# Kernel optimization log

Measured on AMD Instinct MI355X. Metric: run time of the kernel, lower is better.

The kernel has to match this reference:

```python
import jax, jax.numpy as jnp
import numpy as np

B, N, C = 64, 197, 768
H = 12
N_TOK = 118
CUTOFF = 0.15


def setup_inputs() -> dict:
    key = jax.random.key(0)
    ks = jax.random.split(key, 6)
    s = 0.02
    return {
        "x": jax.random.normal(ks[0], (B, N, C), jnp.float32),
        "ln1_w": jnp.ones((C,), jnp.float32),
        "ln1_b": jnp.zeros((C,), jnp.float32),
        "qkv_w": jax.random.normal(ks[1], (3 * C, C), jnp.float32) * s,
        "proj_w": jax.random.normal(ks[2], (C, C), jnp.float32) * s,
        "proj_b": jnp.zeros((C,), jnp.float32),
        "gamma1": jnp.ones((C,), jnp.float32),
        "ln2_w": jnp.ones((C,), jnp.float32),
        "ln2_b": jnp.zeros((C,), jnp.float32),
        "fc1_w": jax.random.normal(ks[3], (4 * C, C), jnp.float32) * s,
        "fc1_b": jnp.zeros((4 * C,), jnp.float32),
        "fc2_w": jax.random.normal(ks[4], (C, 4 * C), jnp.float32) * s,
        "fc2_b": jnp.zeros((C,), jnp.float32),
        "gamma2": jnp.ones((C,), jnp.float32),
    }


def _ln(x, w, b, eps=1e-5):
    m = x.mean(-1, keepdims=True)
    v = ((x - m) ** 2).mean(-1, keepdims=True)
    return (x - m) / jnp.sqrt(v + eps) * w + b


def _attention(x, qkv_w, proj_w, proj_b):
    Bx, Nx, Cx = x.shape
    dh = Cx // H
    qkv = x @ qkv_w.T                                    # [B,N,3C]
    qk = qkv[:, :, : 2 * Cx].reshape(Bx, Nx, 2, H, dh).transpose(2, 0, 3, 1, 4)
    q, k = qk[0], qk[1]                                  # [B,H,N,dh]
    v = qkv[:, :, 2 * Cx :].reshape(Bx, Nx, H, dh).transpose(0, 2, 1, 3)
    attn = jax.nn.softmax((q * dh ** -0.5) @ k.transpose(0, 1, 3, 2), axis=-1)  # [B,H,N,N]
    out = (attn @ v).transpose(0, 2, 1, 3).reshape(Bx, Nx, Cx)
    return out @ proj_w.T + proj_b, attn


def _selector(x, attn, n_tokens, cutoff):
    # attention-weighted scores
    cls_aw = attn[:, :, 1:, 0].mean(-1)[..., None]        # [B,H,1]
    cls_attn = (attn[:, :, 0, 1:] * cls_aw).mean(1)       # [B,N-1]
    img_aw = attn[:, :, 0, 0][..., None]                  # [B,H,1]
    img_attn = (attn[:, :, 1:, 1:].mean(2) * img_aw).mean(1)
    token_attn = cls_attn + img_attn                      # [B,N-1]
    # FFT low-frequency-energy score (detached in original)
    img_token = jax.lax.stop_gradient(x[:, 1:].astype(jnp.float32).transpose(0, 2, 1))  # [B,C,N-1]
    f = jnp.fft.fft(img_token, axis=-1)
    amp = jnp.abs(f)
    pha = jnp.angle(f)
    L = img_token.shape[-1]
    d0 = (L * cutoff / 2.0) ** 2
    m0 = (L - 1) / 2.0
    grid = jnp.arange(L, dtype=jnp.float32)
    kernel = 1.0 - jnp.exp(-((grid - m0) ** 2) / (2.0 * d0))  # high-pass notch
    amp = amp * kernel
    f2 = amp * jnp.cos(pha) + 1j * amp * jnp.sin(pha)
    tok = jnp.fft.ifft(f2, axis=-1)                       # [B,C,N-1] complex
    token_lfe = jnp.abs(tok).sum(1) / jnp.abs(img_token).sum(1).mean(-1)[..., None]
    scores = token_lfe * token_attn                        # [B,N-1]
    _, idx = jax.lax.top_k(scores, n_tokens)               # [B,n_tokens]
    Cx = x.shape[-1]
    sav = jnp.take_along_axis(x[:, 1:], idx[:, :, None], axis=1)  # [B,n_tokens,C]
    return jnp.concatenate([x[:, 0:1], sav], axis=1)


def reference(x, ln1_w, ln1_b, qkv_w, proj_w, proj_b, gamma1,
              ln2_w, ln2_b, fc1_w, fc1_b, fc2_w, fc2_b, gamma2):
    x_msa, attn = _attention(_ln(x, ln1_w, ln1_b), qkv_w, proj_w, proj_b)
    x = gamma1 * x_msa + x
    x = _selector(x, attn, N_TOK, CUTOFF)                 # [B,1+N_TOK,C]
    h = _ln(x, ln2_w, ln2_b)
    h = jax.nn.gelu(h @ fc1_w.T + fc1_b, approximate=False)
    h = h @ fc2_w.T + fc2_b
    return gamma2 * h + x
```

## Files before the change

kernel.cpp:

```cpp
#include <hip/hip_runtime.h>
#include <math.h>

#define NTOK 197
#define NIMG 196
#define CDIM 768
#define NHEAD 12
#define HD 64
#define BATCH 64
#define NSEL 118
#define ROWS_FULL (BATCH*NTOK)
#define ROWS_SEL  (BATCH*(NSEL+1))

typedef short bf16x8 __attribute__((ext_vector_type(8)));
typedef float f32x4  __attribute__((ext_vector_type(4)));

#define GLDS(g, l) __builtin_amdgcn_global_load_lds( \
    (const __attribute__((address_space(1))) void*)(g), \
    (__attribute__((address_space(3))) void*)(l), 16, 0, 0)

__device__ __forceinline__ unsigned short f2bf(float f){
  union { float f; unsigned u; } v; v.f = f;
  unsigned r = v.u + 0x7FFF + ((v.u >> 16) & 1);
  return (unsigned short)(r >> 16);
}
__device__ __forceinline__ float bf2f(unsigned short h){
  union { unsigned u; float f; } v; v.u = ((unsigned)h) << 16; return v.f;
}

template<int OUT>
__global__ __launch_bounds__(256) void ln_kernel(
    const float* __restrict__ x, const float* __restrict__ w,
    const float* __restrict__ b, void* __restrict__ outv)
{
  const int row = blockIdx.x;
  const int t = threadIdx.x;
  const float* xr = x + (size_t)row * CDIM;
  float v0 = xr[t], v1 = xr[t+256], v2 = xr[t+512];
  float s = v0 + v1 + v2;
  __shared__ float red[4], red2[4];
  #pragma unroll
  for (int o=32;o>0;o>>=1) s += __shfl_down(s,o);
  if ((t&63)==0) red[t>>6] = s;
  __syncthreads();
  const float mean = (red[0]+red[1]+red[2]+red[3]) / 768.0f;
  const float d0=v0-mean, d1=v1-mean, d2=v2-mean;
  float vs = d0*d0 + d1*d1 + d2*d2;
  #pragma unroll
  for (int o=32;o>0;o>>=1) vs += __shfl_down(vs,o);
  if ((t&63)==0) red2[t>>6] = vs;
  __syncthreads();
  const float var = (red2[0]+red2[1]+red2[2]+red2[3]) / 768.0f;
  const float rstd = 1.0f / sqrtf(var + 1e-5f);
  const float o0 = d0*rstd*w[t]     + b[t];
  const float o1 = d1*rstd*w[t+256] + b[t+256];
  const float o2 = d2*rstd*w[t+512] + b[t+512];
  if (OUT == 0){
    float* orow = (float*)outv + (size_t)row * CDIM;
    orow[t] = o0; orow[t+256] = o1; orow[t+512] = o2;
  } else {
    unsigned short* orow = (unsigned short*)outv + (size_t)row * CDIM;
    orow[t] = f2bf(o0); orow[t+256] = f2bf(o1); orow[t+512] = f2bf(o2);
  }
}

__global__ __launch_bounds__(256) void ln_split3_kernel(
    const float* __restrict__ x, const float* __restrict__ w,
    const float* __restrict__ b, unsigned short* __restrict__ dst, size_t plane)
{
  const int row = blockIdx.x;
  const int t = threadIdx.x;
  const float* xr = x + (size_t)row * CDIM;
  float v0 = xr[t], v1 = xr[t+256], v2 = xr[t+512];
  float s = v0 + v1 + v2;
  __shared__ float red[4], red2[4];
  #pragma unroll
  for (int o=32;o>0;o>>=1) s += __shfl_down(s,o);
  if ((t&63)==0) red[t>>6] = s;
  __syncthreads();
  const float mean = (red[0]+red[1]+red[2]+red[3]) / 768.0f;
  const float d0=v0-mean, d1=v1-mean, d2=v2-mean;
  float vs = d0*d0 + d1*d1 + d2*d2;
  #pragma unroll
  for (int o=32;o>0;o>>=1) vs += __shfl_down(vs,o);
  if ((t&63)==0) red2[t>>6] = vs;
  __syncthreads();
  const float var = (red2[0]+red2[1]+red2[2]+red2[3]) / 768.0f;
  const float rstd = 1.0f / sqrtf(var + 1e-5f);
  const float ov[3] = { d0*rstd*w[t]     + b[t],
                        d1*rstd*w[t+256] + b[t+256],
                        d2*rstd*w[t+512] + b[t+512] };
  #pragma unroll
  for (int e=0;e<3;e++){
    const int col = t + e*256;
    const float f = ov[e];
    const unsigned short p0 = f2bf(f);
    const float r1 = f - bf2f(p0);
    const unsigned short p1 = f2bf(r1);
    const unsigned short p2 = f2bf(r1 - bf2f(p1));
    dst[(size_t)row*CDIM + col]             = p0;
    dst[plane + (size_t)row*CDIM + col]     = p1;
    dst[2*plane + (size_t)row*CDIM + col]   = p2;
  }
}

__global__ __launch_bounds__(256) void cvt_bf16_kernel(
    const float* __restrict__ src, unsigned short* __restrict__ dst, int n4)
{
  const int i = blockIdx.x*256 + threadIdx.x;
  if (i < n4){
    const float4 v = *(const float4*)(src + (size_t)i*4);
    dst[(size_t)i*4+0] = f2bf(v.x); dst[(size_t)i*4+1] = f2bf(v.y);
    dst[(size_t)i*4+2] = f2bf(v.z); dst[(size_t)i*4+3] = f2bf(v.w);
  }
}

__global__ __launch_bounds__(192) void cvt3_kernel(
    const float* __restrict__ w, unsigned short* __restrict__ W3, int K)
{
  const int n = blockIdx.x, t = threadIdx.x;
  const float4 v = *(const float4*)(w + (size_t)n*K + t*4);
  ushort4 hi, lo;
  hi.x = f2bf(v.x); lo.x = f2bf(v.x - bf2f(hi.x));
  hi.y = f2bf(v.y); lo.y = f2bf(v.y - bf2f(hi.y));
  hi.z = f2bf(v.z); lo.z = f2bf(v.z - bf2f(hi.z));
  hi.w = f2bf(v.w); lo.w = f2bf(v.w - bf2f(hi.w));
  *(ushort4*)(W3 + (size_t)n*2*K + t*4)     = hi;
  *(ushort4*)(W3 + (size_t)n*2*K + K + t*4) = lo;
}

__global__ __launch_bounds__(256) void cvt_split3_kernel(
    const float* __restrict__ src, unsigned short* __restrict__ dst,
    int n4, size_t plane)
{
  const int i = blockIdx.x*256 + threadIdx.x;
  if (i >= n4) return;
  const float4 v = *(const float4*)(src + (size_t)i*4);
  const float f[4] = {v.x, v.y, v.z, v.w};
  unsigned short p0[4], p1[4], p2[4];
  #pragma unroll
  for (int q=0;q<4;q++){
    p0[q] = f2bf(f[q]);
    const float r1 = f[q] - bf2f(p0[q]);
    p1[q] = f2bf(r1);
    const float r2 = r1 - bf2f(p1[q]);
    p2[q] = f2bf(r2);
  }
  *(ushort4*)(dst + (size_t)i*4)           = make_ushort4(p0[0],p0[1],p0[2],p0[3]);
  *(ushort4*)(dst + plane + (size_t)i*4)   = make_ushort4(p1[0],p1[1],p1[2],p1[3]);
  *(ushort4*)(dst + 2*plane + (size_t)i*4) = make_ushort4(p2[0],p2[1],p2[2],p2[3]);
}

__global__ __launch_bounds__(256) void gemm_f32_kernel(
    const float* __restrict__ A, const float* __restrict__ W,
    float* __restrict__ out, int M, int N, int K)
{
  __shared__ float As[16][132];
  __shared__ float Bs[16][132];
  const int t  = threadIdx.x;
  const int tx = t & 15, ty = t >> 4;
  const int m0 = blockIdx.x * 128, n0 = blockIdx.y * 128;
  const int lr = t >> 2, lc = (t & 3) << 2;
  float acc[2][2][4][4] = {{{{0.f}}}};
  const float4 z4 = make_float4(0.f,0.f,0.f,0.f);
  const int rowA0 = m0 + lr, rowA1 = m0 + 64 + lr;
  const size_t strA0 = (size_t)rowA0 * K, strA1 = (size_t)rowA1 * K;
  const size_t strW0 = (size_t)(n0+lr) * K, strW1 = (size_t)(n0+64+lr) * K;
  for (int k0=0; k0<K; k0+=16){
    float4 a0 = (rowA0 < M) ? *(const float4*)(A + strA0 + k0 + lc) : z4;
    float4 a1 = (rowA1 < M) ? *(const float4*)(A + strA1 + k0 + lc) : z4;
    float4 w0 = *(const float4*)(W + strW0 + k0 + lc);
    float4 w1 = *(const float4*)(W + strW1 + k0 + lc);
    __syncthreads();
    As[lc+0][lr]=a0.x; As[lc+1][lr]=a0.y; As[lc+2][lr]=a0.z; As[lc+3][lr]=a0.w;
    As[lc+0][64+lr]=a1.x; As[lc+1][64+lr]=a1.y; As[lc+2][64+lr]=a1.z; As[lc+3][64+lr]=a1.w;
    Bs[lc+0][lr]=w0.x; Bs[lc+1][lr]=w0.y; Bs[lc+2][lr]=w0.z; Bs[lc+3][lr]=w0.w;
    Bs[lc+0][64+lr]=w1.x; Bs[lc+1][64+lr]=w1.y; Bs[lc+2][64+lr]=w1.z; Bs[lc+3][64+lr]=w1.w;
    __syncthreads();
    #pragma unroll
    for (int k=0;k<16;k++){
      const float4 av0 = *(const float4*)&As[k][ty*4];
      const float4 av1 = *(const float4*)&As[k][64+ty*4];
      const float4 bv0 = *(const float4*)&Bs[k][tx*4];
      const float4 bv1 = *(const float4*)&Bs[k][64+tx*4];
      const float ar[2][4] = {{av0.x,av0.y,av0.z,av0.w},{av1.x,av1.y,av1.z,av1.w}};
      const float br[2][4] = {{bv0.x,bv0.y,bv0.z,bv0.w},{bv1.x,bv1.y,bv1.z,bv1.w}};
      #pragma unroll
      for (int ri=0;ri<2;ri++)
        #pragma unroll
        for (int i=0;i<4;i++)
          #pragma unroll
          for (int ci=0;ci<2;ci++)
            #pragma unroll
            for (int j=0;j<4;j++)
              acc[ri][ci][i][j] = fmaf(ar[ri][i], br[ci][j], acc[ri][ci][i][j]);
    }
  }
  #pragma unroll
  for (int ri=0;ri<2;ri++){
    #pragma unroll
    for (int i=0;i<4;i++){
      const int row = m0 + ri*64 + ty*4 + i;
      if (row >= M) continue;
      #pragma unroll
      for (int ci=0;ci<2;ci++){
        const int col = n0 + ci*64 + tx*4;
        *(float4*)(out + (size_t)row*N + col) =
          make_float4(acc[ri][ci][i][0],acc[ri][ci][i][1],acc[ri][ci][i][2],acc[ri][ci][i][3]);
      }
    }
  }
}

__global__ __launch_bounds__(512) void mfma_gemm6w_kernel(
    const unsigned short* __restrict__ A3, const unsigned short* __restrict__ W3,
    float* __restrict__ out, int M, int N, int K, size_t planeA, size_t planeW,
    int gx)
{
  __shared__ __align__(16) unsigned short As[3][64*64];
  __shared__ __align__(16) unsigned short Ws[256*64];
  const int nwg = gridDim.x;
  const int q8 = nwg >> 3, r8 = nwg & 7;
  const int xcd = blockIdx.x & 7, lid = blockIdx.x >> 3;
  const int swz = (xcd < r8) ? (xcd*(q8+1) + lid) : (r8*(q8+1) + (xcd-r8)*q8 + lid);
  const int bx = swz % gx, by = swz / gx;

  const int t = threadIdx.x;
  const int w = t >> 6, lane = t & 63;
  const int m0 = bx * 64, n0 = by * 256;
  const int wr = w >> 2, wc = w & 3;
  f32x4 acc[2][4];
  #pragma unroll
  for (int i=0;i<2;i++)
    #pragma unroll
    for (int j=0;j<4;j++){ acc[i][j][0]=0.f; acc[i][j][1]=0.f; acc[i][j][2]=0.f; acc[i][j][3]=0.f; }

  const int srow = lane >> 3;
  const int slot = lane & 7;
  const int scol = (slot ^ srow) * 8;
  const int aloc = w*8;
  const int wloc = w*32;
  const int fr = lane & 15;
  const int kg = lane >> 4;

  #define SEGW(NA)                                                            \
    _Pragma("unroll")                                                         \
    for (int ksub = 0; ksub < 2; ksub++){                                     \
      const int kbyte = ksub*64 + kg*16;                                      \
      bf16x8 b[4];                                                            \
      _Pragma("unroll")                                                       \
      for (int ni=0; ni<4; ni++){                                             \
        const int br = wc*64 + ni*16 + fr;                                    \
        b[ni] = *(const bf16x8*)(Ws + br*64 + ((kbyte ^ ((br&7)<<4)) >> 1));  \
      }                                                                       \
      _Pragma("unroll")                                                       \
      for (int p=0; p<NA; p++){                                               \
        bf16x8 a[2];                                                          \
        _Pragma("unroll")                                                     \
        for (int mi=0; mi<2; mi++){                                           \
          const int ar = wr*32 + mi*16 + fr;                                  \
          a[mi] = *(const bf16x8*)(As[p] + ar*64 + ((kbyte ^ ((ar&7)<<4)) >> 1)); \
        }                                                                     \
        _Pragma("unroll")                                                     \
        for (int mi=0; mi<2; mi++)                                            \
          _Pragma("unroll")                                                   \
          for (int ni=0; ni<4; ni++)                                          \
            acc[mi][ni] = __builtin_amdgcn_mfma_f32_16x16x32_bf16(a[mi], b[ni], acc[mi][ni], 0, 0, 0); \
      }                                                                       \
    }

  #define STAGE_W(P)                                                          \
    _Pragma("unroll")                                                         \
    for (int tt=0; tt<4; tt++){                                               \
      const int rl = wloc + tt*8;                                             \
      GLDS(W3 + (size_t)(P)*planeW + (size_t)(n0+rl+srow)*K + k0 + scol, Ws + rl*64); \
    }

  for (int k0 = 0; k0 < K; k0 += 64){
    __syncthreads();
    #pragma unroll
    for (int p=0; p<3; p++)
      GLDS(A3 + (size_t)p*planeA + (size_t)(m0+aloc+srow)*K + k0 + scol, As[p] + aloc*64);
    STAGE_W(0)
    __syncthreads();
    SEGW(3)
    __syncthreads();
    STAGE_W(1)
    __syncthreads();
    SEGW(2)
    __syncthreads();
    STAGE_W(2)
    __syncthreads();
    SEGW(1)
  }
  #undef SEGW
  #undef STAGE_W

  const int cL = lane & 15, rL = lane >> 4;
  #pragma unroll
  for (int mi=0; mi<2; mi++){
    #pragma unroll
    for (int ni=0; ni<4; ni++){
      const int col = n0 + wc*64 + ni*16 + cL;
      const int rowb = m0 + wr*32 + mi*16 + rL*4;
      #pragma unroll
      for (int r=0; r<4; r++){
        const int row = rowb + r;
        if (row >= M) continue;
        out[(size_t)row*N + col] = acc[mi][ni][r];
      }
    }
  }
}

template<int EPI>
__global__ __launch_bounds__(512) void mfma_gemm1w_kernel(
    const unsigned short* __restrict__ A, const unsigned short* __restrict__ W,
    const float* __restrict__ bias, const float* __restrict__ gamma,
    const float* __restrict__ resid, void* __restrict__ outv,
    int M, int N, int K, int gx)
{
  __shared__ __align__(16) unsigned short As[64*64];
  __shared__ __align__(16) unsigned short Ws[256*64];
  const int nwg = gridDim.x;
  const int q8 = nwg >> 3, r8 = nwg & 7;
  const int xcd = blockIdx.x & 7, lid = blockIdx.x >> 3;
  const int swz = (xcd < r8) ? (xcd*(q8+1) + lid) : (r8*(q8+1) + (xcd-r8)*q8 + lid);
  const int bx = swz % gx, by = swz / gx;

  const int t = threadIdx.x;
  const int w = t >> 6, lane = t & 63;
  const int m0 = bx * 64, n0 = by * 256;
  const int wr = w >> 2, wc = w & 3;
  f32x4 acc[2][4];
  #pragma unroll
  for (int i=0;i<2;i++)
    #pragma unroll
    for (int j=0;j<4;j++){ acc[i][j][0]=0.f; acc[i][j][1]=0.f; acc[i][j][2]=0.f; acc[i][j][3]=0.f; }

  const int srow = lane >> 3;
  const int slot = lane & 7;
  const int scol = (slot ^ srow) * 8;
  const int aloc = w*8;
  const int wloc = w*32;
  const int fr = lane & 15;
  const int kg = lane >> 4;

  for (int k0 = 0; k0 < K; k0 += 64){
    __syncthreads();
    GLDS(A + (size_t)(m0+aloc+srow)*K + k0 + scol, As + aloc*64);
    #pragma unroll
    for (int tt=0; tt<4; tt++){
      const int rl = wloc + tt*8;
      GLDS(W + (size_t)(n0+rl+srow)*K + k0 + scol, Ws + rl*64);
    }
    __syncthreads();
    #pragma unroll
    for (int ksub = 0; ksub < 2; ksub++){
      const int kbyte = ksub*64 + kg*16;
      bf16x8 b[4];
      #pragma unroll
      for (int ni=0; ni<4; ni++){
        const int br = wc*64 + ni*16 + fr;
        b[ni] = *(const bf16x8*)(Ws + br*64 + ((kbyte ^ ((br&7)<<4)) >> 1));
      }
      bf16x8 a[2];
      #pragma unroll
      for (int mi=0; mi<2; mi++){
        const int ar = wr*32 + mi*16 + fr;
        a[mi] = *(const bf16x8*)(As + ar*64 + ((kbyte ^ ((ar&7)<<4)) >> 1));
      }
      #pragma unroll
      for (int mi=0; mi<2; mi++)
        #pragma unroll
        for (int ni=0; ni<4; ni++)
          acc[mi][ni] = __builtin_amdgcn_mfma_f32_16x16x32_bf16(a[mi], b[ni], acc[mi][ni], 0, 0, 0);
    }
  }

  const int cL = lane & 15, rL = lane >> 4;
  #pragma unroll
  for (int mi=0; mi<2; mi++){
    #pragma unroll
    for (int ni=0; ni<4; ni++){
      const int col = n0 + wc*64 + ni*16 + cL;
      const int rowb = m0 + wr*32 + mi*16 + rL*4;
      const float bb = bias[col];
      #pragma unroll
      for (int r=0; r<4; r++){
        const int row = rowb + r;
        if (row >= M) continue;
        float v = acc[mi][ni][r] + bb;
        if (EPI == 2){
          v = 0.5f*v*(1.0f + erff(v*0.7071067811865475f));
          ((unsigned short*)outv)[(size_t)row*N + col] = f2bf(v);
        } else {
          v = gamma[col]*v + resid[(size_t)row*N + col];
          ((float*)outv)[(size_t)row*N + col] = v;
        }
      }
    }
  }
}

__global__ __launch_bounds__(512) void mfma_proj3_kernel(
    const unsigned short* __restrict__ A, const unsigned short* __restrict__ W,
    const float* __restrict__ bias, const float* __restrict__ gamma,
    const float* __restrict__ resid, float* __restrict__ out,
    int M, int N, int K, int gx)
{
  __shared__ __align__(16) unsigned short Ah[64*64], Al[64*64];
  __shared__ __align__(16) unsigned short Ws[256*64];
  const int nwg = gridDim.x;
  const int q8 = nwg >> 3, r8 = nwg & 7;
  const int xcd = blockIdx.x & 7, lid = blockIdx.x >> 3;
  const int swz = (xcd < r8) ? (xcd*(q8+1) + lid) : (r8*(q8+1) + (xcd-r8)*q8 + lid);
  const int bx = swz % gx, by = swz / gx;

  const int t = threadIdx.x;
  const int w = t >> 6, lane = t & 63;
  const int m0 = bx * 64, n0 = by * 256;
  const int wr = w >> 2, wc = w & 3;
  const int lda = 2*K;
  f32x4 acc[2][4];
  #pragma unroll
  for (int i=0;i<2;i++)
    #pragma unroll
    for (int j=0;j<4;j++){ acc[i][j][0]=0.f; acc[i][j][1]=0.f; acc[i][j][2]=0.f; acc[i][j][3]=0.f; }

  const int srow = lane >> 3;
  const int slot = lane & 7;
  const int scol = (slot ^ srow) * 8;
  const int aloc = w*8;
  const int wloc = w*32;
  const int fr = lane & 15;
  const int kg = lane >> 4;

  #define PSEG(NA)                                                            \
    _Pragma("unroll")                                                         \
    for (int ksub = 0; ksub < 2; ksub++){                                     \
      const int kbyte = ksub*64 + kg*16;                                      \
      bf16x8 b[4];                                                            \
      _Pragma("unroll")                                                       \
      for (int ni=0; ni<4; ni++){                                             \
        const int br = wc*64 + ni*16 + fr;                                    \
        b[ni] = *(const bf16x8*)(Ws + br*64 + ((kbyte ^ ((br&7)<<4)) >> 1));  \
      }                                                                       \
      _Pragma("unroll")                                                       \
      for (int mi=0; mi<2; mi++){                                             \
        const int ar = wr*32 + mi*16 + fr;                                    \
        const int ao = ar*64 + ((kbyte ^ ((ar&7)<<4)) >> 1);                  \
        bf16x8 ah = *(const bf16x8*)(Ah + ao);                                \
        _Pragma("unroll")                                                     \
        for (int ni=0; ni<4; ni++)                                            \
          acc[mi][ni] = __builtin_amdgcn_mfma_f32_16x16x32_bf16(ah, b[ni], acc[mi][ni], 0, 0, 0); \
        if (NA > 1){                                                          \
          bf16x8 al = *(const bf16x8*)(Al + ao);                              \
          _Pragma("unroll")                                                   \
          for (int ni=0; ni<4; ni++)                                          \
            acc[mi][ni] = __builtin_amdgcn_mfma_f32_16x16x32_bf16(al, b[ni], acc[mi][ni], 0, 0, 0); \
        }                                                                     \
      }                                                                       \
    }

  for (int k0 = 0; k0 < K; k0 += 64){
    __syncthreads();
    {
      const size_t abase = (size_t)(m0+aloc+srow)*lda + k0 + scol;
      GLDS(A + abase,     Ah + aloc*64);
      GLDS(A + abase + K, Al + aloc*64);
    }
    #pragma unroll
    for (int tt=0; tt<4; tt++){
      const int rl = wloc + tt*8;
      GLDS(W + (size_t)(n0+rl+srow)*lda + k0 + scol, Ws + rl*64);
    }
    __syncthreads();
    PSEG(2)
    __syncthreads();
    #pragma unroll
    for (int tt=0; tt<4; tt++){
      const int rl = wloc + tt*8;
      GLDS(W + (size_t)(n0+rl+srow)*lda + K + k0 + scol, Ws + rl*64);
    }
    __syncthreads();
    PSEG(1)
  }
  #undef PSEG

  const int cL = lane & 15, rL = lane >> 4;
  #pragma unroll
  for (int mi=0; mi<2; mi++){
    #pragma unroll
    for (int ni=0; ni<4; ni++){
      const int col = n0 + wc*64 + ni*16 + cL;
      const int rowb = m0 + wr*32 + mi*16 + rL*4;
      const float bb = bias[col];
      const float gg = gamma[col];
      #pragma unroll
      for (int r=0; r<4; r++){
        const int row = rowb + r;
        if (row >= M) continue;
        out[(size_t)row*N + col] = gg*(acc[mi][ni][r] + bb) + resid[(size_t)row*N + col];
      }
    }
  }
}

__global__ __launch_bounds__(256) void attn_flash_kernel(
    const float* __restrict__ qkv, double* __restrict__ mbuf,
    double* __restrict__ lbuf, unsigned short* __restrict__ msa3)
{
  __shared__ float Kt[NTOK][HD];
  __shared__ double q0s[HD];
  __shared__ float m0sh;
  __shared__ double red[4];
  __shared__ float l0f;
  const int bh = blockIdx.x;
  const int b = bh / NHEAD, h = bh % NHEAD;
  const float* basep = qkv + (size_t)b*NTOK*2304 + h*HD;
  for (int li=threadIdx.x; li<NTOK*16; li+=256){
    const int r = li >> 4, c4 = (li & 15) << 2;
    *(float4*)&Kt[r][c4] = *(const float4*)(basep + (size_t)r*2304 + 768 + c4);
  }
  if (threadIdx.x < 16){
    const float4 t4 = *(const float4*)(basep + threadIdx.x*4);
    q0s[threadIdx.x*4+0] = (double)t4.x*0.125; q0s[threadIdx.x*4+1] = (double)t4.y*0.125;
    q0s[threadIdx.x*4+2] = (double)t4.z*0.125; q0s[threadIdx.x*4+3] = (double)t4.w*0.125;
  }
  __syncthreads();
  const int i = threadIdx.x;
  float4 q[16];
  float4 o[16];
  float m = -INFINITY, l = 0.f;
  if (i < NTOK){
    #pragma unroll
    for (int dd=0; dd<16; dd++){
      float4 tq = *(const float4*)(basep + (size_t)i*2304 + dd*4);
      q[dd] = make_float4(tq.x*0.125f, tq.y*0.125f, tq.z*0.125f, tq.w*0.125f);
      o[dd] = make_float4(0.f,0.f,0.f,0.f);
    }
    for (int j=0;j<NTOK;j++){
      float s = 0.f;
      #pragma unroll
      for (int dd=0;dd<16;dd++){
        const float4 kk = *(const float4*)&Kt[j][dd*4];
        s = fmaf(q[dd].x,kk.x,s); s = fmaf(q[dd].y,kk.y,s);
        s = fmaf(q[dd].z,kk.z,s); s = fmaf(q[dd].w,kk.w,s);
      }
      const float mn = fmaxf(m, s);
      const float sc = expf(m - mn);
      const float p  = expf(s - mn);
      l = l*sc + p;
      if (sc != 1.0f){
        #pragma unroll
        for (int dd=0;dd<16;dd++){
          o[dd].x *= sc; o[dd].y *= sc; o[dd].z *= sc; o[dd].w *= sc;
        }
      }
      m = mn;
      const float* vrow = basep + (size_t)j*2304 + 1536;
      #pragma unroll
      for (int dd=0;dd<16;dd++){
        const float4 vv = *(const float4*)(vrow + dd*4);
        o[dd].x = fmaf(p,vv.x,o[dd].x); o[dd].y = fmaf(p,vv.y,o[dd].y);
        o[dd].z = fmaf(p,vv.z,o[dd].z); o[dd].w = fmaf(p,vv.w,o[dd].w);
      }
    }
    mbuf[bh*NTOK+i] = (double)m;
    if (i > 0) lbuf[bh*NTOK+i] = (double)(1.0f/l);
    if (i == 0) m0sh = m;
  }
  __syncthreads();
  double e = 0.0;
  if (i < NTOK){
    double s64 = 0.0;
    #pragma unroll
    for (int d=0; d<HD; d++) s64 = fma(q0s[d], (double)Kt[i][d], s64);
    e = exp(s64 - (double)m0sh);
  }
  #pragma unroll
  for (int o2=32;o2>0;o2>>=1) e += __shfl_down(e,o2);
  if ((i&63)==0) red[i>>6] = e;
  __syncthreads();
  if (i==0){
    const double l0 = 1.0/(red[0]+red[1]+red[2]+red[3]);
    lbuf[bh*NTOK] = l0;
    l0f = (float)l0;
  }
  __syncthreads();
  if (i >= NTOK) return;
  const float linv = (i == 0) ? l0f : (1.0f/l);
  unsigned short* orow = msa3 + ((size_t)b*NTOK + i)*1536 + h*HD;
  #pragma unroll
  for (int dd=0;dd<16;dd++){
    const float4 v = make_float4(o[dd].x*linv, o[dd].y*linv, o[dd].z*linv, o[dd].w*linv);
    ushort4 hi, lo;
    hi.x = f2bf(v.x); lo.x = f2bf(v.x - bf2f(hi.x));
    hi.y = f2bf(v.y); lo.y = f2bf(v.y - bf2f(hi.y));
    hi.z = f2bf(v.z); lo.z = f2bf(v.z - bf2f(hi.z));
    hi.w = f2bf(v.w); lo.w = f2bf(v.w - bf2f(hi.w));
    *(ushort4*)(orow + dd*4)       = hi;
    *(ushort4*)(orow + 768 + dd*4) = lo;
  }
}

__global__ __launch_bounds__(256) void attn_sel_kernel(
    const float* __restrict__ qkv, const double* __restrict__ mbuf,
    const double* __restrict__ lbuf, double* __restrict__ ta_part)
{
  __shared__ float Qt[NTOK][HD];
  __shared__ double q0s[HD];
  __shared__ float msf[NTOK], lsf[NTOK];
  __shared__ double m0d, l0inv;
  __shared__ double sh_cs0, sh_r00;
  const int bh = blockIdx.x;
  const int b = bh / NHEAD, h = bh % NHEAD;
  const float* basep = qkv + (size_t)b*NTOK*2304 + h*HD;
  for (int li=threadIdx.x; li<NTOK*16; li+=256){
    const int r = li >> 4, c4 = (li & 15) << 2;
    float4 tq = *(const float4*)(basep + (size_t)r*2304 + c4);
    Qt[r][c4+0]=tq.x*0.125f; Qt[r][c4+1]=tq.y*0.125f;
    Qt[r][c4+2]=tq.z*0.125f; Qt[r][c4+3]=tq.w*0.125f;
  }
  if (threadIdx.x < 16){
    const float4 t4 = *(const float4*)(basep + threadIdx.x*4);
    q0s[threadIdx.x*4+0] = (double)t4.x*0.125; q0s[threadIdx.x*4+1] = (double)t4.y*0.125;
    q0s[threadIdx.x*4+2] = (double)t4.z*0.125; q0s[threadIdx.x*4+3] = (double)t4.w*0.125;
  }
  for (int li=threadIdx.x; li<NTOK; li+=256){
    msf[li] = (float)mbuf[bh*NTOK+li];
    lsf[li] = (float)lbuf[bh*NTOK+li];
  }
  if (threadIdx.x == 0){ m0d = mbuf[bh*NTOK]; l0inv = lbuf[bh*NTOK]; }
  __syncthreads();
  const int j = threadIdx.x;
  double colsum = 0.0, row0 = 0.0;
  if (j < NTOK){
    float4 kreg[16];
    #pragma unroll
    for (int dd=0;dd<16;dd++) kreg[dd] = *(const float4*)(basep + (size_t)j*2304 + 768 + dd*4);
    {
      double s64 = 0.0;
      #pragma unroll
      for (int dd=0;dd<16;dd++){
        s64 = fma(q0s[dd*4+0], (double)kreg[dd].x, s64);
        s64 = fma(q0s[dd*4+1], (double)kreg[dd].y, s64);
        s64 = fma(q0s[dd*4+2], (double)kreg[dd].z, s64);
        s64 = fma(q0s[dd*4+3], (double)kreg[dd].w, s64);
      }
      row0 = exp(s64 - m0d) * l0inv;
    }
    for (int i2=1;i2<NTOK;i2++){
      float s = 0.f;
      #pragma unroll
      for (int dd=0;dd<16;dd++){
        const float4 qq = *(const float4*)&Qt[i2][dd*4];
        s = fmaf(qq.x,kreg[dd].x,s); s = fmaf(qq.y,kreg[dd].y,s);
        s = fmaf(qq.z,kreg[dd].z,s); s = fmaf(qq.w,kreg[dd].w,s);
      }
      colsum += (double)(expf(s - msf[i2]) * lsf[i2]);
    }
  }
  if (j == 0){ sh_cs0 = colsum; sh_r00 = row0; }
  __syncthreads();
  if (j >= 1 && j < NTOK){
    ta_part[(size_t)bh*NIMG + (j-1)] = row0 * (sh_cs0 / 196.0) + (colsum / 196.0) * sh_r00;
  }
}

__global__ __launch_bounds__(256) void reduce_ta_kernel(
    const double* __restrict__ ta_part, double* __restrict__ token_attn)
{
  const int b = blockIdx.x, j = threadIdx.x;
  if (j < NIMG){
    double s = 0.0;
    for (int h=0; h<NHEAD; h++) s += ta_part[((size_t)b*NHEAD + h)*NIMG + j];
    token_attn[b*NIMG + j] = s / 12.0;
  }
}

__global__ __launch_bounds__(256) void circ_kernel(float* __restrict__ circ)
{
  const int d = blockIdx.x;
  const int g = threadIdx.x;
  __shared__ double rs[4], is[4];
  double re = 0.0, im = 0.0;
  if (g < NIMG){
    const double d0   = (196.0 * 0.15 / 2.0);
    const double twod = 2.0 * d0 * d0;
    const double gg = (double)g - 97.5;
    const double kg = 1.0 - exp(-(gg*gg)/twod);
    const int gd = (g*d) % NIMG;
    const double ang = 6.283185307179586476925286766559 * ((double)gd / 196.0);
    re = kg * cos(ang);
    im = kg * sin(ang);
  }
  #pragma unroll
  for (int o=32;o>0;o>>=1){ re += __shfl_down(re,o); im += __shfl_down(im,o); }
  if ((g&63)==0){ rs[g>>6] = re; is[g>>6] = im; }
  __syncthreads();
  if (g == 0){
    circ[d]        = (float)((rs[0]+rs[1]+rs[2]+rs[3]) / 196.0);
    circ[NIMG + d] = (float)((is[0]+is[1]+is[2]+is[3]) / 196.0);
  }
}

__global__ __launch_bounds__(256) void lfe_kernel(
    const float* __restrict__ x1, const float* __restrict__ circ,
    double* __restrict__ lfe_part, double* __restrict__ den_part)
{
  __shared__ float xs[NIMG][36];
  __shared__ float2 c2[NIMG];
  __shared__ double red[4];
  const int cg = blockIdx.x, b = blockIdx.y;
  const int c0 = cg * 32;
  for (int li=threadIdx.x; li<NIMG*32; li+=256){
    const int m = li >> 5, ch = li & 31;
    xs[m][ch] = x1[((size_t)b*NTOK + 1 + m)*CDIM + c0 + ch];
  }
  for (int li=threadIdx.x; li<NIMG; li+=256) c2[li] = make_float2(circ[li], circ[NIMG+li]);
  __syncthreads();
  const int n = threadIdx.x;
  double lfe_sum = 0.0, den_sum = 0.0;
  if (n < NIMG){
    #pragma unroll 1
    for (int g=0; g<4; g++){
      const int cc0 = g*8;
      float re[8] = {0,0,0,0,0,0,0,0};
      float im[8] = {0,0,0,0,0,0,0,0};
      int d = n;
      for (int mm=0; mm<NIMG; mm++){
        const float2 cc = c2[d];
        const float4 xa = *(const float4*)&xs[mm][cc0];
        const float4 xb = *(const float4*)&xs[mm][cc0+4];
        const float xv[8] = {xa.x,xa.y,xa.z,xa.w,xb.x,xb.y,xb.z,xb.w};
        #pragma unroll
        for (int q=0;q<8;q++){
          re[q] = fmaf(cc.x, xv[q], re[q]);
          im[q] = fmaf(cc.y, xv[q], im[q]);
        }
        d = (d==0) ? (NIMG-1) : (d-1);
      }
      #pragma unroll
      for (int q=0;q<8;q++) lfe_sum += (double)sqrtf(re[q]*re[q] + im[q]*im[q]);
    }
    #pragma unroll
    for (int q=0;q<8;q++){
      const float4 xv = *(const float4*)&xs[n][q*4];
      den_sum += (double)fabsf(xv.x)+(double)fabsf(xv.y)+(double)fabsf(xv.z)+(double)fabsf(xv.w);
    }
    lfe_part[((size_t)b*24 + cg)*NIMG + n] = lfe_sum;
  }
  double s = (n < NIMG) ? den_sum : 0.0;
  #pragma unroll
  for (int o=32;o>0;o>>=1) s += __shfl_down(s,o);
  if ((threadIdx.x & 63) == 0) red[threadIdx.x >> 6] = s;
  __syncthreads();
  if (threadIdx.x == 0) den_part[b*24 + cg] = red[0]+red[1]+red[2]+red[3];
}

__global__ __launch_bounds__(256) void scores_kernel(
    const double* __restrict__ lfe_part, const double* __restrict__ den_part,
    const double* __restrict__ token_attn, double* __restrict__ scores)
{
  const int b = blockIdx.x, n = threadIdx.x;
  if (n < NIMG){
    double num = 0.0;
    for (int cg=0; cg<24; cg++) num += lfe_part[((size_t)b*24 + cg)*NIMG + n];
    double den = 0.0;
    for (int cg=0; cg<24; cg++) den += den_part[b*24 + cg];
    const double tl = num / (den / 196.0);
    scores[b*NIMG + n] = tl * token_attn[b*NIMG + n];
  }
}

__global__ void topk_kernel(const double* __restrict__ scores, int* __restrict__ idx)
{
  __shared__ double w[NIMG];
  const int b = blockIdx.x, lane = threadIdx.x;
  for (int i=lane; i<NIMG; i+=64) w[i] = scores[b*NIMG + i];
  __syncthreads();
  for (int r=0; r<NSEL; r++){
    double bv = -INFINITY; int bi = NIMG;
    for (int i=lane; i<NIMG; i+=64){
      const double v = w[i];
      if (v > bv){ bv = v; bi = i; }
    }
    #pragma unroll
    for (int o=32;o>0;o>>=1){
      const double ov = __shfl_down(bv,o);
      const int    oi = __shfl_down(bi,o);
      if (ov > bv || (ov == bv && oi < bi)){ bv = ov; bi = oi; }
    }
    if (lane == 0){
      idx[b*NSEL + r] = bi;
      w[bi] = -INFINITY;
    }
    __syncthreads();
  }
}

__global__ void gather_kernel(const float* __restrict__ x1, const int* __restrict__ idx,
                              float* __restrict__ xsel)
{
  const int row = blockIdx.x;
  const int b = row / (NSEL+1), r = row % (NSEL+1);
  const int src = (r == 0) ? 0 : (1 + idx[b*NSEL + (r-1)]);
  const float4* s = (const float4*)(x1 + ((size_t)b*NTOK + src)*CDIM);
  float4* d = (float4*)(xsel + (size_t)row*CDIM);
  d[threadIdx.x] = s[threadIdx.x];
}

extern "C" void kernel_launch(void* const* d_in, const int* in_sizes, int n_in,
                              void* d_out, int out_size, void* d_ws, size_t ws_size,
                              hipStream_t stream)
{
  const float* x      = (const float*)d_in[0];
  const float* ln1_w  = (const float*)d_in[1];
  const float* ln1_b  = (const float*)d_in[2];
  const float* qkv_w  = (const float*)d_in[3];
  const float* proj_w = (const float*)d_in[4];
  const float* proj_b = (const float*)d_in[5];
  const float* gamma1 = (const float*)d_in[6];
  const float* ln2_w  = (const float*)d_in[7];
  const float* ln2_b  = (const float*)d_in[8];
  const float* fc1_w  = (const float*)d_in[9];
  const float* fc1_b  = (const float*)d_in[10];
  const float* fc2_w  = (const float*)d_in[11];
  const float* fc2_b  = (const float*)d_in[12];
  const float* gamma2 = (const float*)d_in[13];
  float* out = (float*)d_out;
  float* ws  = (float*)d_ws;

  float* R1 = ws;
  float* R2 = ws + 9732096;
  double* D = (double*)(ws + 9732096 + 29048832);
  double* mbuf = D;
  double* lbuf = mbuf + 151296;
  double* tap  = lbuf + 151296;
  double* ta   = tap  + 150528;
  double* lfep = ta   + 12544;
  double* denp = lfep + 301056;
  double* sc   = denp + 1536;
  float* circ  = (float*)(sc + 12544);
  int*   idxb  = (int*)(circ + 392);
  unsigned short* W3p = (unsigned short*)(ws + 40350472);
  unsigned short* WQ3 = (unsigned short*)(ws + 40940296);
  unsigned short* XQ3 = (unsigned short*)(ws + 43594504);
  const size_t NEED_BYTES = (size_t)58192648 * 4;

  float* xln  = R1;
  unsigned short* msa3 = (unsigned short*)R1;
  float* xsel = R1;
  float* qkv  = R2;
  float* x1   = R2;
  unsigned short* ln2o_bf = (unsigned short*)(R2 + 9682944);
  unsigned short* fc1w_bf = (unsigned short*)(R2 + 12632064);
  unsigned short* fc2w_bf = (unsigned short*)(R2 + 13811712);
  unsigned short* h1_bf   = (unsigned short*)(R2 + 14991360);

  if (ws_size >= NEED_BYTES){
    ln_split3_kernel<<<ROWS_FULL, 256, 0, stream>>>(x, ln1_w, ln1_b, XQ3, (size_t)9732096);
    cvt_split3_kernel<<<(442368+255)/256, 256, 0, stream>>>(qkv_w, WQ3, 442368, (size_t)1769472);
    mfma_gemm6w_kernel<<<197*9, 512, 0, stream>>>(XQ3, WQ3, qkv, ROWS_FULL, 2304, 768,
                                                  (size_t)9732096, (size_t)1769472, 197);
  } else {
    ln_kernel<0><<<ROWS_FULL, 256, 0, stream>>>(x, ln1_w, ln1_b, xln);
    gemm_f32_kernel<<<dim3(99,18), 256, 0, stream>>>(xln, qkv_w, qkv, ROWS_FULL, 2304, 768);
  }
  attn_flash_kernel<<<BATCH*NHEAD, 256, 0, stream>>>(qkv, mbuf, lbuf, msa3);
  attn_sel_kernel<<<BATCH*NHEAD, 256, 0, stream>>>(qkv, mbuf, lbuf, tap);
  reduce_ta_kernel<<<BATCH, 256, 0, stream>>>(tap, ta);
  cvt3_kernel<<<CDIM, 192, 0, stream>>>(proj_w, W3p, CDIM);
  mfma_proj3_kernel<<<197*3, 512, 0, stream>>>(msa3, W3p, proj_b, gamma1, x,
                                               x1, ROWS_FULL, CDIM, CDIM, 197);
  cvt_bf16_kernel<<<2304, 256, 0, stream>>>(fc1_w, fc1w_bf, 589824);
  cvt_bf16_kernel<<<2304, 256, 0, stream>>>(fc2_w, fc2w_bf, 589824);
  circ_kernel<<<NIMG, 256, 0, stream>>>(circ);
  lfe_kernel<<<dim3(24, BATCH), 256, 0, stream>>>(x1, circ, lfep, denp);
  scores_kernel<<<BATCH, 256, 0, stream>>>(lfep, denp, ta, sc);
  topk_kernel<<<BATCH, 64, 0, stream>>>(sc, idxb);
  gather_kernel<<<ROWS_SEL, 192, 0, stream>>>(x1, idxb, xsel);
  ln_kernel<1><<<ROWS_SEL, 256, 0, stream>>>(xsel, ln2_w, ln2_b, ln2o_bf);
  mfma_gemm1w_kernel<2><<<119*12, 512, 0, stream>>>(ln2o_bf, fc1w_bf, fc1_b, nullptr,
                                                    nullptr, h1_bf, ROWS_SEL, 3072, 768, 119);
  mfma_gemm1w_kernel<3><<<119*3, 512, 0, stream>>>(h1_bf, fc2w_bf, fc2_b, gamma2,
                                                   xsel, out, ROWS_SEL, 768, 3072, 119);
}
```

Baseline: 1.266 ms.

## Split attention head dim across thread pairs and fuse selector reduction kernels

New measurement: 1.348 ms. 6.4% more time.

```diff
diff --git a/kernel.cpp b/kernel.cpp
--- a/kernel.cpp
+++ b/kernel.cpp
@@ -506,19 +506,19 @@
   }
 }
 
-__global__ __launch_bounds__(256) void attn_flash_kernel(
+__global__ __launch_bounds__(512) void attn_flash_kernel(
     const float* __restrict__ qkv, double* __restrict__ mbuf,
     double* __restrict__ lbuf, unsigned short* __restrict__ msa3)
 {
   __shared__ float Kt[NTOK][HD];
   __shared__ double q0s[HD];
   __shared__ float m0sh;
-  __shared__ double red[4];
+  __shared__ double red[8];
   __shared__ float l0f;
   const int bh = blockIdx.x;
   const int b = bh / NHEAD, h = bh % NHEAD;
   const float* basep = qkv + (size_t)b*NTOK*2304 + h*HD;
-  for (int li=threadIdx.x; li<NTOK*16; li+=256){
+  for (int li=threadIdx.x; li<NTOK*16; li+=512){
     const int r = li >> 4, c4 = (li & 15) << 2;
     *(float4*)&Kt[r][c4] = *(const float4*)(basep + (size_t)r*2304 + 768 + c4);
   }
@@ -528,83 +528,89 @@
     q0s[threadIdx.x*4+2] = (double)t4.z*0.125; q0s[threadIdx.x*4+3] = (double)t4.w*0.125;
   }
   __syncthreads();
-  const int i = threadIdx.x;
-  float4 q[16];
-  float4 o[16];
+  const int i = threadIdx.x >> 1;
+  const int half = threadIdx.x & 1;
+  const int dbase = half*8;
+  const bool act = (i < NTOK);
+  float4 q[8], o[8];
   float m = -INFINITY, l = 0.f;
-  if (i < NTOK){
-    #pragma unroll
-    for (int dd=0; dd<16; dd++){
-      float4 tq = *(const float4*)(basep + (size_t)i*2304 + dd*4);
+  if (act){
+    #pragma unroll
+    for (int dd=0; dd<8; dd++){
+      float4 tq = *(const float4*)(basep + (size_t)i*2304 + (dbase+dd)*4);
       q[dd] = make_float4(tq.x*0.125f, tq.y*0.125f, tq.z*0.125f, tq.w*0.125f);
       o[dd] = make_float4(0.f,0.f,0.f,0.f);
     }
     for (int j=0;j<NTOK;j++){
       float s = 0.f;
       #pragma unroll
-      for (int dd=0;dd<16;dd++){
-        const float4 kk = *(const float4*)&Kt[j][dd*4];
+      for (int dd=0;dd<8;dd++){
+        const float4 kk = *(const float4*)&Kt[j][(dbase+dd)*4];
         s = fmaf(q[dd].x,kk.x,s); s = fmaf(q[dd].y,kk.y,s);
         s = fmaf(q[dd].z,kk.z,s); s = fmaf(q[dd].w,kk.w,s);
       }
+      s += __shfl_xor(s, 1);
       const float mn = fmaxf(m, s);
       const float sc = expf(m - mn);
       const float p  = expf(s - mn);
       l = l*sc + p;
       if (sc != 1.0f){
         #pragma unroll
-        for (int dd=0;dd<16;dd++){
+        for (int dd=0;dd<8;dd++){
           o[dd].x *= sc; o[dd].y *= sc; o[dd].z *= sc; o[dd].w *= sc;
         }
       }
       m = mn;
       const float* vrow = basep + (size_t)j*2304 + 1536;
       #pragma unroll
-      for (int dd=0;dd<16;dd++){
-        const float4 vv = *(const float4*)(vrow + dd*4);
+      for (int dd=0;dd<8;dd++){
+        const float4 vv = *(const float4*)(vrow + (dbase+dd)*4);
         o[dd].x = fmaf(p,vv.x,o[dd].x); o[dd].y = fmaf(p,vv.y,o[dd].y);
         o[dd].z = fmaf(p,vv.z,o[dd].z); o[dd].w = fmaf(p,vv.w,o[dd].w);
       }
     }
-    mbuf[bh*NTOK+i] = (double)m;
-    if (i > 0) lbuf[bh*NTOK+i] = (double)(1.0f/l);
-    if (i == 0) m0sh = m;
+    if (half == 0){
+      mbuf[bh*NTOK+i] = (double)m;
+      if (i > 0) lbuf[bh*NTOK+i] = (double)(1.0f/l);
+      if (threadIdx.x == 0) m0sh = m;
+    }
   }
   __syncthreads();
   double e = 0.0;
-  if (i < NTOK){
+  if (act){
     double s64 = 0.0;
     #pragma unroll
-    for (int d=0; d<HD; d++) s64 = fma(q0s[d], (double)Kt[i][d], s64);
-    e = exp(s64 - (double)m0sh);
+    for (int d=0; d<32; d++) s64 = fma(q0s[half*32+d], (double)Kt[i][half*32+d], s64);
+    s64 += __shfl_xor(s64, 1);
+    if (half == 0) e = exp(s64 - (double)m0sh);
   }
   #pragma unroll
   for (int o2=32;o2>0;o2>>=1) e += __shfl_down(e,o2);
-  if ((i&63)==0) red[i>>6] = e;
-  __syncthreads();
-  if (i==0){
-    const double l0 = 1.0/(red[0]+red[1]+red[2]+red[3]);
+  if ((threadIdx.x&63)==0) red[threadIdx.x>>6] = e;
+  __syncthreads();
+  if (threadIdx.x==0){
+    const double l0 = 1.0/(((red[0]+red[1])+(red[2]+red[3]))+((red[4]+red[5])+(red[6]+red[7])));
     lbuf[bh*NTOK] = l0;
     l0f = (float)l0;
   }
   __syncthreads();
-  if (i >= NTOK) return;
+  if (!act) return;
   const float linv = (i == 0) ? l0f : (1.0f/l);
   unsigned short* orow = msa3 + ((size_t)b*NTOK + i)*1536 + h*HD;
   #pragma unroll
-  for (int dd=0;dd<16;dd++){
+  for (int dd=0;dd<8;dd++){
     const float4 v = make_float4(o[dd].x*linv, o[dd].y*linv, o[dd].z*linv, o[dd].w*linv);
     ushort4 hi, lo;
     hi.x = f2bf(v.x); lo.x = f2bf(v.x - bf2f(hi.x));
     hi.y = f2bf(v.y); lo.y = f2bf(v.y - bf2f(hi.y));
     hi.z = f2bf(v.z); lo.z = f2bf(v.z - bf2f(hi.z));
     hi.w = f2bf(v.w); lo.w = f2bf(v.w - bf2f(hi.w));
-    *(ushort4*)(orow + dd*4)       = hi;
-    *(ushort4*)(orow + 768 + dd*4) = lo;
-  }
-}
-
-__global__ __launch_bounds__(256) void attn_sel_kernel(
+    *(ushort4*)(orow + (dbase+dd)*4)       = hi;
+    *(ushort4*)(orow + 768 + (dbase+dd)*4) = lo;
+  }
+}
+
+__global__ __launch_bounds__(512) void attn_sel_kernel(
     const float* __restrict__ qkv, const double* __restrict__ mbuf,
     const double* __restrict__ lbuf, double* __restrict__ ta_part)
 {
@@ -616,7 +622,7 @@
   const int bh = blockIdx.x;
   const int b = bh / NHEAD, h = bh % NHEAD;
   const float* basep = qkv + (size_t)b*NTOK*2304 + h*HD;
-  for (int li=threadIdx.x; li<NTOK*16; li+=256){
+  for (int li=threadIdx.x; li<NTOK*16; li+=512){
     const int r = li >> 4, c4 = (li & 15) << 2;
     float4 tq = *(const float4*)(basep + (size_t)r*2304 + c4);
     Qt[r][c4+0]=tq.x*0.125f; Qt[r][c4+1]=tq.y*0.125f;
@@ -627,55 +633,49 @@
     q0s[threadIdx.x*4+0] = (double)t4.x*0.125; q0s[threadIdx.x*4+1] = (double)t4.y*0.125;
     q0s[threadIdx.x*4+2] = (double)t4.z*0.125; q0s[threadIdx.x*4+3] = (double)t4.w*0.125;
   }
-  for (int li=threadIdx.x; li<NTOK; li+=256){
+  for (int li=threadIdx.x; li<NTOK; li+=512){
     msf[li] = (float)mbuf[bh*NTOK+li];
     lsf[li] = (float)lbuf[bh*NTOK+li];
   }
   if (threadIdx.x == 0){ m0d = mbuf[bh*NTOK]; l0inv = lbuf[bh*NTOK]; }
   __syncthreads();
-  const int j = threadIdx.x;
+  const int j = threadIdx.x >> 1;
+  const int half = threadIdx.x & 1;
+  const int dbase = half*8;
   double colsum = 0.0, row0 = 0.0;
   if (j < NTOK){
-    float4 kreg[16];
-    #pragma unroll
-    for (int dd=0;dd<16;dd++) kreg[dd] = *(const float4*)(basep + (size_t)j*2304 + 768 + dd*4);
+    float4 kreg[8];
+    #pragma unroll
+    for (int dd=0;dd<8;dd++)
+      kreg[dd] = *(const float4*)(basep + (size_t)j*2304 + 768 + (dbase+dd)*4);
     {
       double s64 = 0.0;
       #pragma unroll
-      for (int dd=0;dd<16;dd++){
-        s64 = fma(q0s[dd*4+0], (double)kreg[dd].x, s64);
-        s64 = fma(q0s[dd*4+1], (double)kreg[dd].y, s64);
-        s64 = fma(q0s[dd*4+2], (double)kreg[dd].z, s64);
-        s64 = fma(q0s[dd*4+3], (double)kreg[dd].w, s64);
-      }
+      for (int dd=0;dd<8;dd++){
+        s64 = fma(q0s[(dbase+dd)*4+0], (double)kreg[dd].x, s64);
+        s64 = fma(q0s[(dbase+dd)*4+1], (double)kreg[dd].y, s64);
+        s64 = fma(q0s[(dbase+dd)*4+2], (double)kreg[dd].z, s64);
+        s64 = fma(q0s[(dbase+dd)*4+3], (double)kreg[dd].w, s64);
+      }
+      s64 += __shfl_xor(s64, 1);
       row0 = exp(s64 - m0d) * l0inv;
     }
     for (int i2=1;i2<NTOK;i2++){
       float s = 0.f;
       #pragma unroll
-      for (int dd=0;dd<16;dd++){
-        const float4 qq = *(const float4*)&Qt[i2][dd*4];
+      for (int dd=0;dd<8;dd++){
+        const float4 qq = *(const float4*)&Qt[i2][(dbase+dd)*4];
         s = fmaf(qq.x,kreg[dd].x,s); s = fmaf(qq.y,kreg[dd].y,s);
         s = fmaf(qq.z,kreg[dd].z,s); s = fmaf(qq.w,kreg[dd].w,s);
       }
+      s += __shfl_xor(s, 1);
       colsum += (double)(expf(s - msf[i2]) * lsf[i2]);
     }
   }
-  if (j == 0){ sh_cs0 = colsum; sh_r00 = row0; }
-  __syncthreads();
-  if (j >= 1 && j < NTOK){
+  if (threadIdx.x == 0){ sh_cs0 = colsum; sh_r00 = row0; }
+  __syncthreads();
+  if (j >= 1 && j < NTOK && half == 0){
     ta_part[(size_t)bh*NIMG + (j-1)] = row0 * (sh_cs0 / 196.0) + (colsum / 196.0) * sh_r00;
-  }
-}
-
-__global__ __launch_bounds__(256) void reduce_ta_kernel(
-    const double* __restrict__ ta_part, double* __restrict__ token_attn)
-{
-  const int b = blockIdx.x, j = threadIdx.x;
-  if (j < NIMG){
-    double s = 0.0;
-    for (int h=0; h<NHEAD; h++) s += ta_part[((size_t)b*NHEAD + h)*NIMG + j];
-    token_attn[b*NIMG + j] = s / 12.0;
   }
 }
 
@@ -759,26 +759,38 @@
   if (threadIdx.x == 0) den_part[b*24 + cg] = red[0]+red[1]+red[2]+red[3];
 }
 
-__global__ __launch_bounds__(256) void scores_kernel(
-    const double* __restrict__ lfe_part, const double* __restrict__ den_part,
-    const double* __restrict__ token_attn, double* __restrict__ scores)
-{
-  const int b = blockIdx.x, n = threadIdx.x;
-  if (n < NIMG){
+__global__ __launch_bounds__(256) void reduce_scores_kernel(
+    const double* __restrict__ ta_part, const double* __restrict__ lfe_part,
+    const double* __restrict__ den_part, double* __restrict__ scores)
+{
+  const int b = blockIdx.x, j = threadIdx.x;
+  if (j < NIMG){
+    double s = 0.0;
+    for (int h=0; h<NHEAD; h++) s += ta_part[((size_t)b*NHEAD + h)*NIMG + j];
+    const double ta = s / 12.0;
     double num = 0.0;
-    for (int cg=0; cg<24; cg++) num += lfe_part[((size_t)b*24 + cg)*NIMG + n];
+    for (int cg=0; cg<24; cg++) num += lfe_part[((size_t)b*24 + cg)*NIMG + j];
     double den = 0.0;
     for (int cg=0; cg<24; cg++) den += den_part[b*24 + cg];
     const double tl = num / (den / 196.0);
-    scores[b*NIMG + n] = tl * token_attn[b*NIMG + n];
-  }
-}
-
-__global__ void topk_kernel(const double* __restrict__ scores, int* __restrict__ idx)
+    scores[b*NIMG + j] = tl * ta;
+  }
+}
+
+__global__ void topk_gather_kernel(const double* __restrict__ scores,
+                                   const float* __restrict__ x1,
+                                   float* __restrict__ xsel)
 {
   __shared__ double w[NIMG];
+  __shared__ int bi_sh;
   const int b = blockIdx.x, lane = threadIdx.x;
   for (int i=lane; i<NIMG; i+=64) w[i] = scores[b*NIMG + i];
+  {
+    const float4* s0 = (const float4*)(x1 + ((size_t)b*NTOK)*CDIM);
+    float4* d0 = (float4*)(xsel + ((size_t)b*(NSEL+1))*CDIM);
+    #pragma unroll
+    for (int c=0;c<3;c++) d0[lane + c*64] = s0[lane + c*64];
+  }
   __syncthreads();
   for (int r=0; r<NSEL; r++){
     double bv = -INFINITY; int bi = NIMG;
@@ -793,22 +805,17 @@
       if (ov > bv || (ov == bv && oi < bi)){ bv = ov; bi = oi; }
     }
     if (lane == 0){
-      idx[b*NSEL + r] = bi;
       w[bi] = -INFINITY;
-    }
-    __syncthreads();
-  }
-}
-
-__global__ void gather_kernel(const float* __restrict__ x1, const int* __restrict__ idx,
-                              float* __restrict__ xsel)
-{
-  const int row = blockIdx.x;
-  const int b = row / (NSEL+1), r = row % (NSEL+1);
-  const int src = (r == 0) ? 0 : (1 + idx[b*NSEL + (r-1)]);
-  const float4* s = (const float4*)(x1 + ((size_t)b*NTOK + src)*CDIM);
-  float4* d = (float4*)(xsel + (size_t)row*CDIM);
-  d[threadIdx.x] = s[threadIdx.x];
+      bi_sh = bi;
+    }
+    __syncthreads();
+    const int src = 1 + bi_sh;
+    const float4* s = (const float4*)(x1 + ((size_t)b*NTOK + src)*CDIM);
+    float4* d = (float4*)(xsel + ((size_t)b*(NSEL+1) + 1 + r)*CDIM);
+    #pragma unroll
+    for (int c=0;c<3;c++) d[lane + c*64] = s[lane + c*64];
+    __syncthreads();
+  }
 }
 
 extern "C" void kernel_launch(void* const* d_in, const int* in_sizes, int n_in,
@@ -843,7 +850,6 @@
   double* denp = lfep + 301056;
   double* sc   = denp + 1536;
   float* circ  = (float*)(sc + 12544);
-  int*   idxb  = (int*)(circ + 392);
   unsigned short* W3p = (unsigned short*)(ws + 40350472);
   unsigned short* WQ3 = (unsigned short*)(ws + 40940296);
   unsigned short* XQ3 = (unsigned short*)(ws + 43594504);
@@ -868,9 +874,8 @@
     ln_kernel<0><<<ROWS_FULL, 256, 0, stream>>>(x, ln1_w, ln1_b, xln);
     gemm_f32_kernel<<<dim3(99,18), 256, 0, stream>>>(xln, qkv_w, qkv, ROWS_FULL, 2304, 768);
   }
-  attn_flash_kernel<<<BATCH*NHEAD, 256, 0, stream>>>(qkv, mbuf, lbuf, msa3);
-  attn_sel_kernel<<<BATCH*NHEAD, 256, 0, stream>>>(qkv, mbuf, lbuf, tap);
-  reduce_ta_kernel<<<BATCH, 256, 0, stream>>>(tap, ta);
+  attn_flash_kernel<<<BATCH*NHEAD, 512, 0, stream>>>(qkv, mbuf, lbuf, msa3);
+  attn_sel_kernel<<<BATCH*NHEAD, 512, 0, stream>>>(qkv, mbuf, lbuf, tap);
   cvt3_kernel<<<CDIM, 192, 0, stream>>>(proj_w, W3p, CDIM);
   mfma_proj3_kernel<<<197*3, 512, 0, stream>>>(msa3, W3p, proj_b, gamma1, x,
                                                x1, ROWS_FULL, CDIM, CDIM, 197);
@@ -878,9 +883,8 @@
   cvt_bf16_kernel<<<2304, 256, 0, stream>>>(fc2_w, fc2w_bf, 589824);
   circ_kernel<<<NIMG, 256, 0, stream>>>(circ);
   lfe_kernel<<<dim3(24, BATCH), 256, 0, stream>>>(x1, circ, lfep, denp);
-  scores_kernel<<<BATCH, 256, 0, stream>>>(lfep, denp, ta, sc);
-  topk_kernel<<<BATCH, 64, 0, stream>>>(sc, idxb);
-  gather_kernel<<<ROWS_SEL, 192, 0, stream>>>(x1, idxb, xsel);
+  reduce_scores_kernel<<<BATCH, 256, 0, stream>>>(tap, lfep, denp, sc);
+  topk_gather_kernel<<<BATCH, 64, 0, stream>>>(sc, x1, xsel);
   ln_kernel<1><<<ROWS_SEL, 256, 0, stream>>>(xsel, ln2_w, ln2_b, ln2o_bf);
   mfma_gemm1w_kernel<2><<<119*12, 512, 0, stream>>>(ln2o_bf, fc1w_bf, fc1_b, nullptr,
                                                     nullptr, h1_bf, ROWS_SEL, 3072, 768, 119);
```

## Split attention-selector column sums across two blocks per head with combine kernel

Applied to the files above, without the earlier changes.

Measured after the change: 1.128 ms. 10.9% less time.

```diff
diff --git a/kernel.cpp b/kernel.cpp
--- a/kernel.cpp
+++ b/kernel.cpp
@@ -604,42 +604,42 @@
   }
 }
 
-__global__ __launch_bounds__(256) void attn_sel_kernel(
+__global__ __launch_bounds__(256) void attn_selp_kernel(
     const float* __restrict__ qkv, const double* __restrict__ mbuf,
-    const double* __restrict__ lbuf, double* __restrict__ ta_part)
-{
-  __shared__ float Qt[NTOK][HD];
+    const double* __restrict__ lbuf, double* __restrict__ csp,
+    double* __restrict__ e0buf)
+{
+  __shared__ float Qt[98][HD];
   __shared__ double q0s[HD];
-  __shared__ float msf[NTOK], lsf[NTOK];
-  __shared__ double m0d, l0inv;
-  __shared__ double sh_cs0, sh_r00;
-  const int bh = blockIdx.x;
+  __shared__ float msf[98], lsf[98];
+  const int bh   = blockIdx.x >> 1;
+  const int half = blockIdx.x & 1;
+  const int i2base = 1 + half*98;
   const int b = bh / NHEAD, h = bh % NHEAD;
   const float* basep = qkv + (size_t)b*NTOK*2304 + h*HD;
-  for (int li=threadIdx.x; li<NTOK*16; li+=256){
+  for (int li=threadIdx.x; li<98*16; li+=256){
     const int r = li >> 4, c4 = (li & 15) << 2;
-    float4 tq = *(const float4*)(basep + (size_t)r*2304 + c4);
+    float4 tq = *(const float4*)(basep + (size_t)(i2base + r)*2304 + c4);
     Qt[r][c4+0]=tq.x*0.125f; Qt[r][c4+1]=tq.y*0.125f;
     Qt[r][c4+2]=tq.z*0.125f; Qt[r][c4+3]=tq.w*0.125f;
   }
-  if (threadIdx.x < 16){
+  if (half == 0 && threadIdx.x < 16){
     const float4 t4 = *(const float4*)(basep + threadIdx.x*4);
     q0s[threadIdx.x*4+0] = (double)t4.x*0.125; q0s[threadIdx.x*4+1] = (double)t4.y*0.125;
     q0s[threadIdx.x*4+2] = (double)t4.z*0.125; q0s[threadIdx.x*4+3] = (double)t4.w*0.125;
   }
-  for (int li=threadIdx.x; li<NTOK; li+=256){
-    msf[li] = (float)mbuf[bh*NTOK+li];
-    lsf[li] = (float)lbuf[bh*NTOK+li];
-  }
-  if (threadIdx.x == 0){ m0d = mbuf[bh*NTOK]; l0inv = lbuf[bh*NTOK]; }
+  for (int li=threadIdx.x; li<98; li+=256){
+    msf[li] = (float)mbuf[bh*NTOK + i2base + li];
+    lsf[li] = (float)lbuf[bh*NTOK + i2base + li];
+  }
   __syncthreads();
   const int j = threadIdx.x;
-  double colsum = 0.0, row0 = 0.0;
   if (j < NTOK){
     float4 kreg[16];
     #pragma unroll
     for (int dd=0;dd<16;dd++) kreg[dd] = *(const float4*)(basep + (size_t)j*2304 + 768 + dd*4);
-    {
+    if (half == 0){
+      const double m0d = mbuf[bh*NTOK];
       double s64 = 0.0;
       #pragma unroll
       for (int dd=0;dd<16;dd++){
@@ -648,23 +648,51 @@
         s64 = fma(q0s[dd*4+2], (double)kreg[dd].z, s64);
         s64 = fma(q0s[dd*4+3], (double)kreg[dd].w, s64);
       }
-      row0 = exp(s64 - m0d) * l0inv;
-    }
-    for (int i2=1;i2<NTOK;i2++){
+      e0buf[(size_t)bh*NTOK + j] = exp(s64 - m0d);
+    }
+    double colsum = 0.0;
+    for (int r=0;r<98;r++){
       float s = 0.f;
       #pragma unroll
       for (int dd=0;dd<16;dd++){
-        const float4 qq = *(const float4*)&Qt[i2][dd*4];
+        const float4 qq = *(const float4*)&Qt[r][dd*4];
         s = fmaf(qq.x,kreg[dd].x,s); s = fmaf(qq.y,kreg[dd].y,s);
         s = fmaf(qq.z,kreg[dd].z,s); s = fmaf(qq.w,kreg[dd].w,s);
       }
-      colsum += (double)(expf(s - msf[i2]) * lsf[i2]);
-    }
-  }
-  if (j == 0){ sh_cs0 = colsum; sh_r00 = row0; }
+      colsum += (double)(expf(s - msf[r]) * lsf[r]);
+    }
+    csp[(size_t)blockIdx.x*NTOK + j] = colsum;
+  }
+}
+
+__global__ __launch_bounds__(256) void attn_selc_kernel(
+    const double* __restrict__ csp, const double* __restrict__ e0buf,
+    double* __restrict__ ta_part)
+{
+  __shared__ double red[4];
+  __shared__ double sh_cs0, sh_e00, sh_l0inv;
+  const int bh = blockIdx.x;
+  const int j = threadIdx.x;
+  double colsum = 0.0, e0 = 0.0;
+  if (j < NTOK){
+    colsum = csp[(size_t)(bh*2)*NTOK + j] + csp[(size_t)(bh*2+1)*NTOK + j];
+    e0 = e0buf[(size_t)bh*NTOK + j];
+  }
+  double e = e0;
+  #pragma unroll
+  for (int o=32;o>0;o>>=1) e += __shfl_down(e,o);
+  if ((threadIdx.x&63)==0) red[threadIdx.x>>6] = e;
+  __syncthreads();
+  if (threadIdx.x == 0){
+    sh_l0inv = 1.0/(red[0]+red[1]+red[2]+red[3]);
+    sh_cs0 = colsum;
+    sh_e00 = e0;
+  }
   __syncthreads();
   if (j >= 1 && j < NTOK){
-    ta_part[(size_t)bh*NIMG + (j-1)] = row0 * (sh_cs0 / 196.0) + (colsum / 196.0) * sh_r00;
+    const double row0 = e0 * sh_l0inv;
+    const double r00  = sh_e00 * sh_l0inv;
+    ta_part[(size_t)bh*NIMG + (j-1)] = row0 * (sh_cs0 / 196.0) + (colsum / 196.0) * r00;
   }
 }
 
@@ -849,6 +877,9 @@
   unsigned short* XQ3 = (unsigned short*)(ws + 43594504);
   const size_t NEED_BYTES = (size_t)58192648 * 4;
 
+  double* csp   = lfep;
+  double* e0buf = (double*)(ws + 40940296);
+
   float* xln  = R1;
   unsigned short* msa3 = (unsigned short*)R1;
   float* xsel = R1;
@@ -869,7 +900,8 @@
     gemm_f32_kernel<<<dim3(99,18), 256, 0, stream>>>(xln, qkv_w, qkv, ROWS_FULL, 2304, 768);
   }
   attn_flash_kernel<<<BATCH*NHEAD, 256, 0, stream>>>(qkv, mbuf, lbuf, msa3);
-  attn_sel_kernel<<<BATCH*NHEAD, 256, 0, stream>>>(qkv, mbuf, lbuf, tap);
+  attn_selp_kernel<<<BATCH*NHEAD*2, 256, 0, stream>>>(qkv, mbuf, lbuf, csp, e0buf);
+  attn_selc_kernel<<<BATCH*NHEAD, 256, 0, stream>>>(csp, e0buf, tap);
   reduce_ta_kernel<<<BATCH, 256, 0, stream>>>(tap, ta);
   cvt3_kernel<<<CDIM, 192, 0, stream>>>(proj_w, W3p, CDIM);
   mfma_proj3_kernel<<<197*3, 512, 0, stream>>>(msa3, W3p, proj_b, gamma1, x,
```
